# Optimization experiments

Hardware: AMD Instinct MI355X
Metric: run time of the kernel (lower is better)

## Reference

```python
import jax, jax.numpy as jnp
import numpy as np

C = 1024
H = 16
DH = C // H
T = 2048
B = 2
EPS = 1e-5


def setup_inputs() -> dict:
    key = jax.random.key(0)
    ks = jax.random.split(key, 11)
    s = 1.0 / np.sqrt(C)
    return {
        "x": jax.random.normal(ks[0], (B, C, T), dtype=jnp.float32),
        "Wq": jax.random.normal(ks[1], (C, C), dtype=jnp.float32) * s,
        "bq": jax.random.normal(ks[2], (C,), dtype=jnp.float32) * 0.01,
        "Wk": jax.random.normal(ks[3], (C, C), dtype=jnp.float32) * s,
        "bk": jax.random.normal(ks[4], (C,), dtype=jnp.float32) * 0.01,
        "Wv": jax.random.normal(ks[5], (C, C), dtype=jnp.float32) * s,
        "bv": jax.random.normal(ks[6], (C,), dtype=jnp.float32) * 0.01,
        "Wo": jax.random.normal(ks[7], (C, C), dtype=jnp.float32) * s,
        "bo": jax.random.normal(ks[8], (C,), dtype=jnp.float32) * 0.01,
        "gamma": jax.random.normal(ks[9], (C,), dtype=jnp.float32) * 0.1,
        "beta": jax.random.normal(ks[10], (C,), dtype=jnp.float32) * 0.1,
    }


def reference(x, Wq, bq, Wk, bk, Wv, bv, Wo, bo, gamma, beta):
    scale = DH ** (-0.5)
    # conv1x1 projections: [B,C,T] x [C_out,C_in] -> [B,C,T]
    q = jnp.einsum('bct,dc->bdt', x, Wq) + bq[None, :, None]
    k = jnp.einsum('bct,dc->bdt', x, Wk) + bk[None, :, None]
    v = jnp.einsum('bct,dc->bdt', x, Wv) + bv[None, :, None]
    # split heads: [B,C,T] -> [B,H,Dh,T]
    q = q.reshape(B, H, DH, T).transpose(0, 1, 3, 2) * scale  # [B,H,T,Dh]
    k = k.reshape(B, H, DH, T)                                # [B,H,Dh,T]
    v = v.reshape(B, H, DH, T).transpose(0, 1, 3, 2)          # [B,H,T,Dh]
    sim = jnp.einsum('bhtd,bhds->bhts', q, k)                 # [B,H,T,T]
    attn = jax.nn.softmax(sim, axis=-1)
    attn = jnp.nan_to_num(attn, nan=0.0)
    out = jnp.einsum('bhts,bhsd->bhtd', attn, v)              # [B,H,T,Dh]
    out = out.transpose(0, 1, 3, 2).reshape(B, C, T)          # [B,C,T]
    y = jnp.einsum('bct,dc->bdt', out, Wo) + bo[None, :, None]
    # BatchNorm1d (training mode: batch statistics over B and T)
    mean = jnp.mean(y, axis=(0, 2), keepdims=True)
    var = jnp.var(y, axis=(0, 2), keepdims=True)
    y = (y - mean) * jax.lax.rsqrt(var + EPS)
    y = y * gamma[None, :, None] + beta[None, :, None]
    return x + y
```

## Files before the change

### kernel.cpp

```cpp
#include <hip/hip_runtime.h>

#define CC 1024
#define HH 16
#define DHH 64
#define TT 2048
#define BB 2

typedef short s8v __attribute__((ext_vector_type(8)));
typedef float f32x4 __attribute__((ext_vector_type(4)));

__device__ __forceinline__ unsigned short f2bf(float f) {
    union { float f; unsigned int u; } v; v.f = f;
    unsigned int r = v.u + 0x7FFFu + ((v.u >> 16) & 1u);
    return (unsigned short)(r >> 16);
}

__device__ __forceinline__ float fexp2(float x) {
#if __has_builtin(__builtin_amdgcn_exp2f)
    return __builtin_amdgcn_exp2f(x);
#else
    return exp2f(x);
#endif
}

__device__ __forceinline__ void gl_lds16(const unsigned short* g, unsigned short* l) {
    __builtin_amdgcn_global_load_lds(
        (const __attribute__((address_space(1))) unsigned int*)g,
        (__attribute__((address_space(3))) unsigned int*)l, 16, 0, 0);
}

__device__ __forceinline__ s8v lds_ld(const unsigned short* base, int byteoff) {
    return *(const s8v*)((const char*)base + byteoff);
}

__device__ __forceinline__ int xcd_swz(int orig, int nwg) {
    int cpx = nwg >> 3;
    return (orig & 7) * cpx + (orig >> 3);
}

__global__ void transpose_cast(const float* __restrict__ x, unsigned short* __restrict__ xT) {
    __shared__ float tile[32][33];
    int b = blockIdx.z;
    int t0 = blockIdx.x * 32, c0 = blockIdx.y * 32;
    int tx = threadIdx.x, ty = threadIdx.y;
    const float* xb = x + (size_t)b * CC * TT;
    #pragma unroll
    for (int i = 0; i < 32; i += 8)
        tile[ty + i][tx] = xb[(size_t)(c0 + ty + i) * TT + t0 + tx];
    __syncthreads();
    unsigned short* xTb = xT + (size_t)b * TT * CC;
    #pragma unroll
    for (int i = 0; i < 32; i += 8)
        xTb[(size_t)(t0 + ty + i) * CC + c0 + tx] = f2bf(tile[tx][ty + i]);
}

__global__ void cast_weights(const float* __restrict__ Wq, const float* __restrict__ Wk,
                             const float* __restrict__ Wv, const float* __restrict__ Wo,
                             unsigned short* __restrict__ out) {
    int i = blockIdx.x * 256 + threadIdx.x;
    int which = i >> 18;
    int j = (i & 0x3FFFF) * 4;
    const float* s = (which == 0) ? Wq : (which == 1) ? Wk : (which == 2) ? Wv : Wo;
    float4 v = *(const float4*)(s + j);
    unsigned short* d = out + (size_t)which * 1048576 + j;
    ushort4 pk; pk.x = f2bf(v.x); pk.y = f2bf(v.y); pk.z = f2bf(v.z); pk.w = f2bf(v.w);
    *(ushort4*)d = pk;
}

__device__ __forceinline__ void gemm_core_k1024(
    const unsigned short* __restrict__ A, const unsigned short* __restrict__ Bt,
    unsigned short* As, unsigned short* Bs,
    int m0, int n0, int tid, f32x4 (&acc)[4][4]) {
    const int w = tid >> 6, l = tid & 63;
    const int ln = l & 15, hi = l >> 4;
    const int wm = (w >> 1) * 64, wn = (w & 1) * 64;
    int offA[4], offB[4];
    #pragma unroll
    for (int i = 0; i < 4; ++i) {
        int ra = wm + 16 * i + ln;
        offA[i] = ra * 64 + ((hi ^ ((ra >> 1) & 3)) * 16);
        int rb = wn + 16 * i + ln;
        offB[i] = rb * 64 + ((hi ^ ((rb >> 1) & 3)) * 16);
    }
    auto stage = [&](int buf, int k0) {
        #pragma unroll
        for (int j = 0; j < 2; ++j) {
            int p = j * 256 + tid;
            int r = p >> 2, g = (p & 3) ^ ((r >> 1) & 3);
            gl_lds16(A + (size_t)(m0 + r) * CC + k0 + 8 * g, As + buf * 4096 + (j * 256 + w * 64) * 8);
            gl_lds16(Bt + (size_t)(n0 + r) * CC + k0 + 8 * g, Bs + buf * 4096 + (j * 256 + w * 64) * 8);
        }
    };
    stage(0, 0);
    for (int kk = 0; kk < 32; ++kk) {
        const int cur = kk & 1;
        if (kk < 31) {
            stage(cur ^ 1, (kk + 1) * 32);
            asm volatile("s_waitcnt vmcnt(4)" ::: "memory");
        } else {
            asm volatile("s_waitcnt vmcnt(0)" ::: "memory");
        }
        __builtin_amdgcn_sched_barrier(0);
        __builtin_amdgcn_s_barrier();
        __builtin_amdgcn_sched_barrier(0);
        const unsigned short* Ab = As + cur * 4096;
        const unsigned short* Bb = Bs + cur * 4096;
        s8v a[4], bb[4];
        #pragma unroll
        for (int i = 0; i < 4; ++i) { a[i] = lds_ld(Ab, offA[i]); bb[i] = lds_ld(Bb, offB[i]); }
        __builtin_amdgcn_s_setprio(1);
        #pragma unroll
        for (int i = 0; i < 4; ++i)
            #pragma unroll
            for (int jj = 0; jj < 4; ++jj)
                acc[i][jj] = __builtin_amdgcn_mfma_f32_16x16x32_bf16(a[i], bb[jj], acc[i][jj], 0, 0, 0);
        __builtin_amdgcn_s_setprio(0);
        __builtin_amdgcn_s_barrier();
        __builtin_amdgcn_sched_barrier(0);
    }
}

__global__ __launch_bounds__(256, 3)
void gemm_qkv(const unsigned short* __restrict__ xT, const unsigned short* __restrict__ Wb,
              unsigned short* __restrict__ qTp, unsigned short* __restrict__ kTp,
              unsigned short* __restrict__ vp,
              const float* __restrict__ bq, const float* __restrict__ bk,
              const float* __restrict__ bv, float qscale) {
    __shared__ unsigned short As[2 * 4096];
    __shared__ unsigned short Bs[2 * 4096];
    const int tid = threadIdx.x;
    const int wgid = xcd_swz(blockIdx.x, 768);
    const int z = wgid >> 7, bx = wgid & 127;
    const int which = z >> 1, b = z & 1;
    const long TC = (long)TT * CC;

    const unsigned short* A; const unsigned short* Bt;
    int m0, n0;
    if (which < 2) {
        A = xT + (size_t)b * TC;
        Bt = Wb + (size_t)which * 1048576;
        n0 = (bx & 7) * 128; m0 = (bx >> 3) * 128;
    } else {
        A = Wb + 2097152;
        Bt = xT + (size_t)b * TC;
        n0 = (bx & 15) * 128; m0 = (bx >> 4) * 128;
    }

    f32x4 acc[4][4] = {};
    gemm_core_k1024(A, Bt, As, Bs, m0, n0, tid, acc);

    const int w = tid >> 6, l = tid & 63;
    const int ln = l & 15, hi = l >> 4;
    const int wm = (w >> 1) * 64, wn = (w & 1) * 64;

    if (which < 2) {
        unsigned short* Out = (which == 0 ? qTp : kTp) + (size_t)b * TC;
        const float* bias = (which == 0) ? bq : bk;
        float scale = (which == 0) ? qscale : 1.0f;
        #pragma unroll
        for (int i = 0; i < 4; ++i)
            #pragma unroll
            for (int jj = 0; jj < 4; ++jj) {
                int col = n0 + wn + 16 * jj + ln;
                float bvv = bias[col];
                #pragma unroll
                for (int r = 0; r < 4; ++r) {
                    int row = m0 + wm + 16 * i + hi * 4 + r;
                    Out[(size_t)row * CC + col] = f2bf((acc[i][jj][r] + bvv) * scale);
                }
            }
    } else {
        unsigned short* Out = vp + (size_t)b * TC;
        #pragma unroll
        for (int i = 0; i < 4; ++i)
            #pragma unroll
            for (int r = 0; r < 4; ++r) {
                int row = m0 + wm + 16 * i + hi * 4 + r;
                float bvv = bv[row];
                #pragma unroll
                for (int jj = 0; jj < 4; ++jj) {
                    int col = n0 + wn + 16 * jj + ln;
                    Out[(size_t)row * TT + col] = f2bf(acc[i][jj][r] + bvv);
                }
            }
    }
}

__global__ __launch_bounds__(256, 2)
void gemm_y(const unsigned short* __restrict__ Wo, const unsigned short* __restrict__ outT,
            float* __restrict__ y, const float* __restrict__ bo) {
    __shared__ unsigned short As[2 * 4096];
    __shared__ unsigned short Bs[2 * 4096];
    const int tid = threadIdx.x;
    const int wgid = xcd_swz(blockIdx.x, 256);
    const int b = wgid >> 7, bx = wgid & 127;
    const int n0 = (bx & 15) * 128, m0 = (bx >> 4) * 128;
    const long TC = (long)TT * CC;

    f32x4 acc[4][4] = {};
    gemm_core_k1024(Wo, outT + (size_t)b * TC, As, Bs, m0, n0, tid, acc);

    const int w = tid >> 6, l = tid & 63;
    const int ln = l & 15, hi = l >> 4;
    const int wm = (w >> 1) * 64, wn = (w & 1) * 64;
    float* Out = y + (size_t)b * TC;
    #pragma unroll
    for (int i = 0; i < 4; ++i)
        #pragma unroll
        for (int r = 0; r < 4; ++r) {
            int row = m0 + wm + 16 * i + hi * 4 + r;
            float bvv = bo[row];
            #pragma unroll
            for (int jj = 0; jj < 4; ++jj) {
                int col = n0 + wn + 16 * jj + ln;
                Out[(size_t)row * TT + col] = acc[i][jj][r] + bvv;
            }
        }
}

__global__ __launch_bounds__(256, 2)
void attn_kernel(const unsigned short* __restrict__ qT,
                 const unsigned short* __restrict__ kT,
                 const unsigned short* __restrict__ vv,
                 unsigned short* __restrict__ oT) {
    __shared__ unsigned short Ks[2][128 * 64];
    __shared__ unsigned short Vs[2][64 * 128];

    const int tid = threadIdx.x;
    const int w = tid >> 6, l = tid & 63;
    const int ln = l & 15, hi = l >> 4;
    const int wgid = xcd_swz(blockIdx.x, 512);
    const int qt0 = (wgid & 15) * 128;
    const int bh = wgid >> 4;
    const int b = bh >> 4, h = bh & 15;
    const size_t bTT = (size_t)b * TT;

    auto stageKV = [&](int buf, int kt) {
        #pragma unroll
        for (int j = 0; j < 4; ++j) {
            int p = j * 256 + tid;
            int r = p >> 3, g = (p & 7) ^ (r & 7);
            gl_lds16(kT + (bTT + kt + r) * CC + h * DHH + 8 * g, &Ks[buf][(j * 256 + w * 64) * 8]);
        }
        #pragma unroll
        for (int j = 0; j < 4; ++j) {
            int p = j * 256 + tid;
            int r = p >> 4, g = (p & 15) ^ (r & 7);
            gl_lds16(vv + ((size_t)b * CC + h * DHH + r) * TT + kt + 8 * g, &Vs[buf][(j * 256 + w * 64) * 8]);
        }
    };

    stageKV(0, 0);

    s8v qf[2][2];
    {
        const unsigned short* qbase = qT + (bTT + qt0 + w * 32) * CC + h * DHH;
        #pragma unroll
        for (int rf = 0; rf < 2; ++rf)
            #pragma unroll
            for (int kc = 0; kc < 2; ++kc)
                qf[rf][kc] = *(const s8v*)(qbase + (size_t)(rf * 16 + ln) * CC + kc * 32 + 8 * hi);
    }

    f32x4 of[2][4] = {};
    float mi[2] = {-1e30f, -1e30f};
    float li[2] = {0.f, 0.f};

    int fidx[4];
    #pragma unroll
    for (int r = 0; r < 4; ++r) fidx[r] = (l & 48) | (hi * 4 + r);

    for (int ti = 0; ti < 16; ++ti) {
        const int cur = ti & 1;
        if (ti < 15) {
            stageKV(cur ^ 1, (ti + 1) * 128);
            asm volatile("s_waitcnt vmcnt(8)" ::: "memory");
        } else {
            asm volatile("s_waitcnt vmcnt(0)" ::: "memory");
        }
        __builtin_amdgcn_sched_barrier(0);
        __builtin_amdgcn_s_barrier();
        __builtin_amdgcn_sched_barrier(0);

        const unsigned short* Kb = &Ks[cur][0];
        const unsigned short* Vb = &Vs[cur][0];

        f32x4 sf[2][8];
        #pragma unroll
        for (int cf = 0; cf < 8; ++cf) {
            int rk = cf * 16 + ln;
            s8v k0 = lds_ld(Kb, rk * 128 + ((hi ^ (rk & 7)) * 16));
            s8v k1 = lds_ld(Kb, rk * 128 + (((4 + hi) ^ (rk & 7)) * 16));
            __builtin_amdgcn_s_setprio(1);
            #pragma unroll
            for (int rf = 0; rf < 2; ++rf) {
                f32x4 t = (f32x4){0.f, 0.f, 0.f, 0.f};
                t = __builtin_amdgcn_mfma_f32_16x16x32_bf16(k0, qf[rf][0], t, 0, 0, 0);
                t = __builtin_amdgcn_mfma_f32_16x16x32_bf16(k1, qf[rf][1], t, 0, 0, 0);
                sf[rf][cf] = t;
            }
            __builtin_amdgcn_s_setprio(0);
        }

        unsigned int pw[2][8][2];
        #pragma unroll
        for (int rf = 0; rf < 2; ++rf) {
            float m4[8];
            #pragma unroll
            for (int cf = 0; cf < 8; ++cf)
                m4[cf] = fmaxf(fmaxf(sf[rf][cf][0], sf[rf][cf][1]),
                               fmaxf(sf[rf][cf][2], sf[rf][cf][3]));
            float mx = fmaxf(fmaxf(fmaxf(m4[0], m4[1]), fmaxf(m4[2], m4[3])),
                             fmaxf(fmaxf(m4[4], m4[5]), fmaxf(m4[6], m4[7])));
            mx = fmaxf(mx, __shfl_xor(mx, 16));
            mx = fmaxf(mx, __shfl_xor(mx, 32));
            float fac = 1.0f;
            if (__any(mx > mi[rf] + 8.0f)) {
                float mn = fmaxf(mi[rf], mx);
                fac = fexp2(mi[rf] - mn);
                mi[rf] = mn;
                float facr[4];
                #pragma unroll
                for (int r = 0; r < 4; ++r) facr[r] = __shfl(fac, fidx[r]);
                #pragma unroll
                for (int nf = 0; nf < 4; ++nf)
                    #pragma unroll
                    for (int r = 0; r < 4; ++r) of[rf][nf][r] *= facr[r];
            }
            float mn = mi[rf];
            float ps0 = 0.f, ps1 = 0.f, ps2 = 0.f, ps3 = 0.f;
            #pragma unroll
            for (int cf = 0; cf < 8; ++cf) {
                float p0 = fexp2(sf[rf][cf][0] - mn);
                float p1 = fexp2(sf[rf][cf][1] - mn);
                float p2 = fexp2(sf[rf][cf][2] - mn);
                float p3 = fexp2(sf[rf][cf][3] - mn);
                ps0 += p0; ps1 += p1; ps2 += p2; ps3 += p3;
                unsigned int w0, w1;
                asm("v_cvt_pk_bf16_f32 %0, %1, %2" : "=v"(w0) : "v"(p0), "v"(p1));
                asm("v_cvt_pk_bf16_f32 %0, %1, %2" : "=v"(w1) : "v"(p2), "v"(p3));
                pw[rf][cf][0] = w0;
                pw[rf][cf][1] = w1;
            }
            float ps = (ps0 + ps1) + (ps2 + ps3);
            ps += __shfl_xor(ps, 16);
            ps += __shfl_xor(ps, 32);
            li[rf] = li[rf] * fac + ps;
        }

        #pragma unroll
        for (int kc = 0; kc < 4; ++kc) {
            s8v pa[2];
            #pragma unroll
            for (int rf = 0; rf < 2; ++rf) {
                unsigned int A0 = pw[rf][2 * kc][0], B0 = pw[rf][2 * kc + 1][0];
                unsigned int A1 = pw[rf][2 * kc][1], B1 = pw[rf][2 * kc + 1][1];
                asm("v_permlane32_swap_b32 %0, %1" : "+v"(A0), "+v"(B0));
                asm("v_permlane16_swap_b32 %0, %1" : "+v"(A0), "+v"(B0));
                asm("v_permlane32_swap_b32 %0, %1" : "+v"(A1), "+v"(B1));
                asm("v_permlane16_swap_b32 %0, %1" : "+v"(A1), "+v"(B1));
                union { unsigned int u[4]; s8v v; } up;
                up.u[0] = A0; up.u[1] = A1; up.u[2] = B0; up.u[3] = B1;
                pa[rf] = up.v;
            }
            __builtin_amdgcn_s_setprio(1);
            #pragma unroll
            for (int nf = 0; nf < 4; ++nf) {
                int rv = nf * 16 + ln;
                s8v vb = lds_ld(Vb, rv * 256 + (((kc * 4 + hi) ^ (rv & 7)) * 16));
                #pragma unroll
                for (int rf = 0; rf < 2; ++rf)
                    of[rf][nf] = __builtin_amdgcn_mfma_f32_16x16x32_bf16(pa[rf], vb, of[rf][nf], 0, 0, 0);
            }
            __builtin_amdgcn_s_setprio(0);
        }
        __builtin_amdgcn_s_barrier();
        __builtin_amdgcn_sched_barrier(0);
    }

    #pragma unroll
    for (int rf = 0; rf < 2; ++rf) {
        float inv = 1.0f / li[rf];
        float invr[4];
        #pragma unroll
        for (int r = 0; r < 4; ++r) invr[r] = __shfl(inv, fidx[r]);
        #pragma unroll
        for (int nf = 0; nf < 4; ++nf)
            #pragma unroll
            for (int r = 0; r < 4; ++r) {
                int row = qt0 + w * 32 + rf * 16 + hi * 4 + r;
                int col = h * DHH + nf * 16 + ln;
                oT[(bTT + row) * CC + col] = f2bf(of[rf][nf][r] * invr[r]);
            }
    }
}

__global__ void bn_stats(const float* __restrict__ y, float* __restrict__ mean,
                         float* __restrict__ rstd) {
    int c = blockIdx.x;
    float s = 0.f, ss = 0.f;
    for (int b = 0; b < BB; ++b) {
        const float* row = y + ((size_t)b * CC + c) * TT;
        for (int t = threadIdx.x; t < TT; t += 256) {
            float v = row[t];
            s += v; ss += v * v;
        }
    }
    #pragma unroll
    for (int m = 1; m < 64; m <<= 1) { s += __shfl_xor(s, m); ss += __shfl_xor(ss, m); }
    __shared__ float a1[4], a2[4];
    int w = threadIdx.x >> 6;
    if ((threadIdx.x & 63) == 0) { a1[w] = s; a2[w] = ss; }
    __syncthreads();
    if (threadIdx.x == 0) {
        s = a1[0] + a1[1] + a1[2] + a1[3];
        ss = a2[0] + a2[1] + a2[2] + a2[3];
        const float inv_n = 1.0f / (BB * TT);
        float mu = s * inv_n;
        float var = ss * inv_n - mu * mu;
        mean[c] = mu;
        rstd[c] = rsqrtf(var + 1e-5f);
    }
}

__global__ void final_out(const float* __restrict__ x, const float* __restrict__ y,
                          const float* __restrict__ mean, const float* __restrict__ rstd,
                          const float* __restrict__ gamma, const float* __restrict__ beta,
                          float* __restrict__ out) {
    int row = blockIdx.x;
    int c = row & (CC - 1);
    float a = gamma[c] * rstd[c];
    float bb = beta[c] - mean[c] * a;
    size_t base = (size_t)row * TT;
    for (int t = threadIdx.x * 4; t < TT; t += 256 * 4) {
        float4 xv = *(const float4*)(x + base + t);
        float4 yv = *(const float4*)(y + base + t);
        float4 o;
        o.x = xv.x + a * yv.x + bb;
        o.y = xv.y + a * yv.y + bb;
        o.z = xv.z + a * yv.z + bb;
        o.w = xv.w + a * yv.w + bb;
        *(float4*)(out + base + t) = o;
    }
}

extern "C" void kernel_launch(void* const* d_in, const int* in_sizes, int n_in,
                              void* d_out, int out_size, void* d_ws, size_t ws_size,
                              hipStream_t stream) {
    const float* x     = (const float*)d_in[0];
    const float* Wq    = (const float*)d_in[1];
    const float* bq    = (const float*)d_in[2];
    const float* Wk    = (const float*)d_in[3];
    const float* bk    = (const float*)d_in[4];
    const float* Wv    = (const float*)d_in[5];
    const float* bv    = (const float*)d_in[6];
    const float* Wo    = (const float*)d_in[7];
    const float* bo    = (const float*)d_in[8];
    const float* gamma = (const float*)d_in[9];
    const float* beta  = (const float*)d_in[10];
    float* out = (float*)d_out;

    char* ws = (char*)d_ws;
    unsigned short* buf0 = (unsigned short*)(ws);
    unsigned short* Wb   = (unsigned short*)(ws + 8388608);
    unsigned short* qTp  = (unsigned short*)(ws + 16777216);
    unsigned short* kTp  = (unsigned short*)(ws + 25165824);
    unsigned short* vp   = (unsigned short*)(ws + 33554432);
    float* yp            = (float*)(ws + 16777216);
    float* meanp         = (float*)(ws + 41943040);
    float* rstdp         = (float*)(ws + 41947136);

    transpose_cast<<<dim3(TT / 32, CC / 32, BB), dim3(32, 8), 0, stream>>>(x, buf0);
    cast_weights<<<dim3(4096), dim3(256), 0, stream>>>(Wq, Wk, Wv, Wo, Wb);

    gemm_qkv<<<dim3(768), dim3(256), 0, stream>>>(
        buf0, Wb, qTp, kTp, vp, bq, bk, bv, 0.125f * 1.4426950408889634f);

    attn_kernel<<<dim3(512), dim3(256), 0, stream>>>(qTp, kTp, vp, buf0);

    gemm_y<<<dim3(256), dim3(256), 0, stream>>>(Wb + 3145728, buf0, yp, bo);

    bn_stats<<<dim3(CC), dim3(256), 0, stream>>>(yp, meanp, rstdp);
    final_out<<<dim3(BB * CC), dim3(256), 0, stream>>>(x, yp, meanp, rstdp, gamma, beta, out);
}
```

Before: 138.4 us.

## Use 8 waves per attention block, each owning 16 query rows

The attention kernel now launches 512 threads per block, so each of 8 waves handles 16 query rows instead of 32. This cuts per-wave register state (S tile, O accumulator, softmax stats) so more waves fit per CU, and K/V staging is spread over more threads. K LDS offsets and global staging pointers are precomputed and advanced incrementally, in both the GEMM core and attention, to save address arithmetic. The trade-off is that each K/V fragment read from LDS now feeds half as many MFMAs, which raises LDS traffic per unit of compute.

```diff
diff --git a/kernel.cpp b/kernel.cpp
--- a/kernel.cpp
+++ b/kernel.cpp
@@ -82,20 +82,29 @@
         int rb = wn + 16 * i + ln;
         offB[i] = rb * 64 + ((hi ^ ((rb >> 1) & 3)) * 16);
     }
-    auto stage = [&](int buf, int k0) {
+    const unsigned short* ap[2];
+    const unsigned short* bp[2];
+    #pragma unroll
+    for (int j = 0; j < 2; ++j) {
+        int p = j * 256 + tid;
+        int r = p >> 2, g = (p & 3) ^ ((r >> 1) & 3);
+        ap[j] = A + (size_t)(m0 + r) * CC + 8 * g;
+        bp[j] = Bt + (size_t)(n0 + r) * CC + 8 * g;
+    }
+    auto stage = [&](int buf) {
         #pragma unroll
         for (int j = 0; j < 2; ++j) {
-            int p = j * 256 + tid;
-            int r = p >> 2, g = (p & 3) ^ ((r >> 1) & 3);
-            gl_lds16(A + (size_t)(m0 + r) * CC + k0 + 8 * g, As + buf * 4096 + (j * 256 + w * 64) * 8);
-            gl_lds16(Bt + (size_t)(n0 + r) * CC + k0 + 8 * g, Bs + buf * 4096 + (j * 256 + w * 64) * 8);
-        }
+            gl_lds16(ap[j], As + buf * 4096 + (j * 256 + w * 64) * 8);
+            gl_lds16(bp[j], Bs + buf * 4096 + (j * 256 + w * 64) * 8);
+        }
+        #pragma unroll
+        for (int j = 0; j < 2; ++j) { ap[j] += 32; bp[j] += 32; }
     };
-    stage(0, 0);
+    stage(0);
     for (int kk = 0; kk < 32; ++kk) {
         const int cur = kk & 1;
         if (kk < 31) {
-            stage(cur ^ 1, (kk + 1) * 32);
+            stage(cur ^ 1);
             asm volatile("s_waitcnt vmcnt(4)" ::: "memory");
         } else {
             asm volatile("s_waitcnt vmcnt(0)" ::: "memory");
@@ -218,7 +227,7 @@
         }
 }
 
-__global__ __launch_bounds__(256, 2)
+__global__ __launch_bounds__(512, 4)
 void attn_kernel(const unsigned short* __restrict__ qT,
                  const unsigned short* __restrict__ kT,
                  const unsigned short* __restrict__ vv,
@@ -235,37 +244,47 @@
     const int b = bh >> 4, h = bh & 15;
     const size_t bTT = (size_t)b * TT;
 
-    auto stageKV = [&](int buf, int kt) {
-        #pragma unroll
-        for (int j = 0; j < 4; ++j) {
-            int p = j * 256 + tid;
-            int r = p >> 3, g = (p & 7) ^ (r & 7);
-            gl_lds16(kT + (bTT + kt + r) * CC + h * DHH + 8 * g, &Ks[buf][(j * 256 + w * 64) * 8]);
-        }
-        #pragma unroll
-        for (int j = 0; j < 4; ++j) {
-            int p = j * 256 + tid;
-            int r = p >> 4, g = (p & 15) ^ (r & 7);
-            gl_lds16(vv + ((size_t)b * CC + h * DHH + r) * TT + kt + 8 * g, &Vs[buf][(j * 256 + w * 64) * 8]);
-        }
+    const unsigned short* kp[2];
+    const unsigned short* vp2[2];
+    #pragma unroll
+    for (int j = 0; j < 2; ++j) {
+        int c = j * 512 + tid;
+        int rk = c >> 3, gk = (c & 7) ^ (rk & 7);
+        kp[j] = kT + (bTT + rk) * CC + h * DHH + 8 * gk;
+        int rv = c >> 4, gv = (c & 15) ^ (rv & 7);
+        vp2[j] = vv + ((size_t)b * CC + h * DHH + rv) * TT + 8 * gv;
+    }
+    auto stage = [&](int buf) {
+        #pragma unroll
+        for (int j = 0; j < 2; ++j)
+            gl_lds16(kp[j], &Ks[buf][(j * 512 + w * 64) * 8]);
+        #pragma unroll
+        for (int j = 0; j < 2; ++j)
+            gl_lds16(vp2[j], &Vs[buf][(j * 512 + w * 64) * 8]);
+        #pragma unroll
+        for (int j = 0; j < 2; ++j) { kp[j] += 128 * CC; vp2[j] += 128; }
     };
 
-    stageKV(0, 0);
-
-    s8v qf[2][2];
+    stage(0);
+
+    s8v qf[2];
     {
-        const unsigned short* qbase = qT + (bTT + qt0 + w * 32) * CC + h * DHH;
-        #pragma unroll
-        for (int rf = 0; rf < 2; ++rf)
-            #pragma unroll
-            for (int kc = 0; kc < 2; ++kc)
-                qf[rf][kc] = *(const s8v*)(qbase + (size_t)(rf * 16 + ln) * CC + kc * 32 + 8 * hi);
-    }
-
-    f32x4 of[2][4] = {};
-    float mi[2] = {-1e30f, -1e30f};
-    float li[2] = {0.f, 0.f};
-
+        const unsigned short* qbase = qT + (bTT + qt0 + w * 16 + ln) * CC + h * DHH;
+        #pragma unroll
+        for (int kc = 0; kc < 2; ++kc)
+            qf[kc] = *(const s8v*)(qbase + kc * 32 + 8 * hi);
+    }
+
+    int koff[8][2];
+    #pragma unroll
+    for (int cf = 0; cf < 8; ++cf) {
+        int rk = cf * 16 + ln;
+        koff[cf][0] = rk * 128 + ((hi ^ (rk & 7)) * 16);
+        koff[cf][1] = rk * 128 + (((4 + hi) ^ (rk & 7)) * 16);
+    }
+
+    f32x4 of[4] = {};
+    float mi = -1e30f, li = 0.f;
     int fidx[4];
     #pragma unroll
     for (int r = 0; r < 4; ++r) fidx[r] = (l & 48) | (hi * 4 + r);
@@ -273,8 +292,8 @@
     for (int ti = 0; ti < 16; ++ti) {
         const int cur = ti & 1;
         if (ti < 15) {
-            stageKV(cur ^ 1, (ti + 1) * 128);
-            asm volatile("s_waitcnt vmcnt(8)" ::: "memory");
+            stage(cur ^ 1);
+            asm volatile("s_waitcnt vmcnt(4)" ::: "memory");
         } else {
             asm volatile("s_waitcnt vmcnt(0)" ::: "memory");
         }
@@ -285,102 +304,93 @@
         const unsigned short* Kb = &Ks[cur][0];
         const unsigned short* Vb = &Vs[cur][0];
 
-        f32x4 sf[2][8];
+        f32x4 sf[8];
         #pragma unroll
         for (int cf = 0; cf < 8; ++cf) {
-            int rk = cf * 16 + ln;
-            s8v k0 = lds_ld(Kb, rk * 128 + ((hi ^ (rk & 7)) * 16));
-            s8v k1 = lds_ld(Kb, rk * 128 + (((4 + hi) ^ (rk & 7)) * 16));
+            s8v k0 = lds_ld(Kb, koff[cf][0]);
+            s8v k1 = lds_ld(Kb, koff[cf][1]);
             __builtin_amdgcn_s_setprio(1);
-            #pragma unroll
-            for (int rf = 0; rf < 2; ++rf) {
-                f32x4 t = (f32x4){0.f, 0.f, 0.f, 0.f};
-                t = __builtin_amdgcn_mfma_f32_16x16x32_bf16(k0, qf[rf][0], t, 0, 0, 0);
-                t = __builtin_amdgcn_mfma_f32_16x16x32_bf16(k1, qf[rf][1], t, 0, 0, 0);
-                sf[rf][cf] = t;
-            }
+            f32x4 t = (f32x4){0.f, 0.f, 0.f, 0.f};
+            t = __builtin_amdgcn_mfma_f32_16x16x32_bf16(k0, qf[0], t, 0, 0, 0);
+            t = __builtin_amdgcn_mfma_f32_16x16x32_bf16(k1, qf[1], t, 0, 0, 0);
+            sf[cf] = t;
             __builtin_amdgcn_s_setprio(0);
         }
 
-        unsigned int pw[2][8][2];
-        #pragma unroll
-        for (int rf = 0; rf < 2; ++rf) {
+        unsigned int pw[8][2];
+        {
             float m4[8];
             #pragma unroll
             for (int cf = 0; cf < 8; ++cf)
-                m4[cf] = fmaxf(fmaxf(sf[rf][cf][0], sf[rf][cf][1]),
-                               fmaxf(sf[rf][cf][2], sf[rf][cf][3]));
+                m4[cf] = fmaxf(fmaxf(sf[cf][0], sf[cf][1]), fmaxf(sf[cf][2], sf[cf][3]));
             float mx = fmaxf(fmaxf(fmaxf(m4[0], m4[1]), fmaxf(m4[2], m4[3])),
                              fmaxf(fmaxf(m4[4], m4[5]), fmaxf(m4[6], m4[7])));
             mx = fmaxf(mx, __shfl_xor(mx, 16));
             mx = fmaxf(mx, __shfl_xor(mx, 32));
             float fac = 1.0f;
-            if (__any(mx > mi[rf] + 8.0f)) {
-                float mn = fmaxf(mi[rf], mx);
-                fac = fexp2(mi[rf] - mn);
-                mi[rf] = mn;
+            if (__any(mx > mi + 8.0f)) {
+                float mn = fmaxf(mi, mx);
+                fac = fexp2(mi - mn);
+                mi = mn;
                 float facr[4];
                 #pragma unroll
                 for (int r = 0; r < 4; ++r) facr[r] = __shfl(fac, fidx[r]);
                 #pragma unroll
                 for (int nf = 0; nf < 4; ++nf)
                     #pragma unroll
-                    for (int r = 0; r < 4; ++r) of[rf][nf][r] *= facr[r];
-            }
-            float mn = mi[rf];
+                    for (int r = 0; r < 4; ++r) of[nf][r] *= facr[r];
+            }
+            float mn = mi;
             float ps0 = 0.f, ps1 = 0.f, ps2 = 0.f, ps3 = 0.f;
             #pragma unroll
             for (int cf = 0; cf < 8; ++cf) {
-                float p0 = fexp2(sf[rf][cf][0] - mn);
-                float p1 = fexp2(sf[rf][cf][1] - mn);
-                float p2 = fexp2(sf[rf][cf][2] - mn);
-                float p3 = fexp2(sf[rf][cf][3] - mn);
+                float p0 = fexp2(sf[cf][0] - mn);
+                float p1 = fexp2(sf[cf][1] - mn);
+                float p2 = fexp2(sf[cf][2] - mn);
+                float p3 = fexp2(sf[cf][3] - mn);
                 ps0 += p0; ps1 += p1; ps2 += p2; ps3 += p3;
                 unsigned int w0, w1;
                 asm("v_cvt_pk_bf16_f32 %0, %1, %2" : "=v"(w0) : "v"(p0), "v"(p1));
                 asm("v_cvt_pk_bf16_f32 %0, %1, %2" : "=v"(w1) : "v"(p2), "v"(p3));
-                pw[rf][cf][0] = w0;
-                pw[rf][cf][1] = w1;
+                pw[cf][0] = w0;
+                pw[cf][1] = w1;
             }
             float ps = (ps0 + ps1) + (ps2 + ps3);
             ps += __shfl_xor(ps, 16);
             ps += __shfl_xor(ps, 32);
-            li[rf] = li[rf] * fac + ps;
+            li = li * fac + ps;
         }
 
         #pragma unroll
         for (int kc = 0; kc < 4; ++kc) {
-            s8v pa[2];
-            #pragma unroll
-            for (int rf = 0; rf < 2; ++rf) {
-                unsigned int A0 = pw[rf][2 * kc][0], B0 = pw[rf][2 * kc + 1][0];
-                unsigned int A1 = pw[rf][2 * kc][1], B1 = pw[rf][2 * kc + 1][1];
+            s8v pa;
+            {
+                unsigned int A0 = pw[2 * kc][0], B0 = pw[2 * kc + 1][0];
+                unsigned int A1 = pw[2 * kc][1], B1 = pw[2 * kc + 1][1];
                 asm("v_permlane32_swap_b32 %0, %1" : "+v"(A0), "+v"(B0));
                 asm("v_permlane16_swap_b32 %0, %1" : "+v"(A0), "+v"(B0));
                 asm("v_permlane32_swap_b32 %0, %1" : "+v"(A1), "+v"(B1));
                 asm("v_permlane16_swap_b32 %0, %1" : "+v"(A1), "+v"(B1));
                 union { unsigned int u[4]; s8v v; } up;
                 up.u[0] = A0; up.u[1] = A1; up.u[2] = B0; up.u[3] = B1;
-                pa[rf] = up.v;
+                pa = up.v;
             }
             __builtin_amdgcn_s_setprio(1);
             #pragma unroll
             for (int nf = 0; nf < 4; ++nf) {
                 int rv = nf * 16 + ln;
                 s8v vb = lds_ld(Vb, rv * 256 + (((kc * 4 + hi) ^ (rv & 7)) * 16));
-                #pragma unroll
-                for (int rf = 0; rf < 2; ++rf)
-                    of[rf][nf] = __builtin_amdgcn_mfma_f32_16x16x32_bf16(pa[rf], vb, of[rf][nf], 0, 0, 0);
+                of[nf] = __builtin_amdgcn_mfma_f32_16x16x32_bf16(pa, vb, of[nf], 0, 0, 0);
             }
             __builtin_amdgcn_s_setprio(0);
         }
+        __builtin_amdgcn_sched_barrier(0);
         __builtin_amdgcn_s_barrier();
         __builtin_amdgcn_sched_barrier(0);
     }
 
-    #pragma unroll
-    for (int rf = 0; rf < 2; ++rf) {
-        float inv = 1.0f / li[rf];
+    {
+        float inv = 1.0f / li;
         float invr[4];
         #pragma unroll
         for (int r = 0; r < 4; ++r) invr[r] = __shfl(inv, fidx[r]);
@@ -388,9 +398,9 @@
         for (int nf = 0; nf < 4; ++nf)
             #pragma unroll
             for (int r = 0; r < 4; ++r) {
-                int row = qt0 + w * 32 + rf * 16 + hi * 4 + r;
+                int row = qt0 + w * 16 + hi * 4 + r;
                 int col = h * DHH + nf * 16 + ln;
-                oT[(bTT + row) * CC + col] = f2bf(of[rf][nf][r] * invr[r]);
+                oT[(bTT + row) * CC + col] = f2bf(of[nf][r] * invr[r]);
             }
     }
 }
@@ -476,7 +486,7 @@
     gemm_qkv<<<dim3(768), dim3(256), 0, stream>>>(
         buf0, Wb, qTp, kTp, vp, bq, bk, bv, 0.125f * 1.4426950408889634f);
 
-    attn_kernel<<<dim3(512), dim3(256), 0, stream>>>(qTp, kTp, vp, buf0);
+    attn_kernel<<<dim3(512), dim3(512), 0, stream>>>(qTp, kTp, vp, buf0);
 
     gemm_y<<<dim3(256), dim3(256), 0, stream>>>(Wb + 3145728, buf0, yp, bo);
 
```

After: 133.4 us. -3.6%, faster.
